# Kernel tuning notes

Hardware: AMD Instinct MI355X
Metric: run time of the kernel (lower is better)

## Reference

```python
import jax, jax.numpy as jnp
import numpy as np

H, W, S = 480, 1024, 32
MULT_THRESH, ADD_THRESH = 0.01, 0.1


def setup_inputs() -> dict:
    key = jax.random.key(0)
    k1, k2 = jax.random.split(key)
    flows_f = jax.random.normal(k1, (1, S, 2, H, W), jnp.float32)
    noise = jax.random.normal(k2, (1, S, 2, H, W), jnp.float32)
    # near-inverse backward flow so the fwd-bwd consistency check passes for many points
    flows_b = -flows_f + 0.05 * noise
    return {"flows_f": flows_f, "flows_b": flows_b, "margin": 10, "sample_step": 4}


def bilinear_sample(im, x, y):
    # im: (C,H,W); x,y: (N,) float pixel coords -> (C,N). Matches torch bilinear_sample2d
    # (weights from unclipped coords, gather indices clipped to the image).
    C, Hh, Ww = im.shape
    x0 = jnp.floor(x); y0 = jnp.floor(y)
    wx1 = x - x0; wx0 = 1.0 - wx1
    wy1 = y - y0; wy0 = 1.0 - wy1
    x0i = jnp.clip(x0.astype(jnp.int32), 0, Ww - 1)
    x1i = jnp.clip(x0i + 1, 0, Ww - 1)
    y0i = jnp.clip(y0.astype(jnp.int32), 0, Hh - 1)
    y1i = jnp.clip(y0i + 1, 0, Hh - 1)
    g = lambda yi, xi: im[:, yi, xi]  # (C,N)
    return (g(y0i, x0i) * (wy0 * wx0) + g(y0i, x1i) * (wy0 * wx1)
            + g(y1i, x0i) * (wy1 * wx0) + g(y1i, x1i) * (wy1 * wx1))


def _forward(ff, fb, margin, sample_step):
    # ff, fb: (S, 2, H, W) forward / backward flows (batch squeezed, B=1)
    gy = jnp.arange(margin, H - margin + 1, sample_step, dtype=jnp.float32)
    gx = jnp.arange(margin, W - margin + 1, sample_step, dtype=jnp.float32)
    YY, XX = jnp.meshgrid(gy, gx, indexing='ij')
    ys_g = YY.reshape(-1); xs_g = XX.reshape(-1)          # (G,) base sampling grid
    G = xs_g.shape[0]
    N = 2 * H * W // (sample_step ** 2)                   # trajectory slot capacity
    R = min(N, G)                                         # max births per step (static)

    by, bx = jnp.meshgrid(jnp.arange(H, dtype=jnp.float32),
                          jnp.arange(W, dtype=jnp.float32), indexing='ij')

    def prune(flow_f, flow_b):
        # fwd-bwd consistency mask 'on': (H,W) in {0,1}
        xt = (bx + flow_f[0]).reshape(-1)
        yt = (by + flow_f[1]).reshape(-1)
        fbw = bilinear_sample(flow_b, xt, yt).reshape(2, H, W)  # backwarped bwd flow
        diff = jnp.sqrt(jnp.sum((flow_f + fbw) ** 2, axis=0))
        mag = 0.5 * (jnp.sqrt(jnp.sum(flow_f ** 2, axis=0)) + jnp.sqrt(jnp.sum(fbw ** 2, axis=0)))
        return (diff <= MULT_THRESH * mag + ADD_THRESH).astype(jnp.float32)

    X = jnp.zeros((S, N), jnp.float32)
    Y = jnp.zeros((S, N), jnp.float32)
    Start = -jnp.ones((N,), jnp.float32)
    X = X.at[0, :G].set(xs_g)
    Y = Y.at[0, :G].set(ys_g)
    Start = Start.at[:G].set(0.0)

    def step(carry, inp):
        X, Y, Start = carry
        flow_f, flow_b, s = inp
        on = prune(flow_f, flow_b)                         # (H,W)
        active = Start >= 0.0                              # (N,) live-slot mask (replaces where(Start>=0))
        xs_o = X[s]; ys_o = Y[s]
        uv = bilinear_sample(flow_f, xs_o, ys_o)           # (2,N) flow at current points
        xs_t = xs_o + uv[0]; ys_t = ys_o + uv[1]
        fb_ok = bilinear_sample(on[None], xs_o, ys_o)[0] > 0.5
        marg = ((xs_t > margin) & (ys_t > margin) &
                (xs_t < W - margin) & (ys_t < H - margin))
        choose = active & marg & fb_ok
        # scatter surviving points into row s+1 (row starts as zeros, matching init)
        X = X.at[s + 1].set(jnp.where(choose, xs_t, 0.0))
        Y = Y.at[s + 1].set(jnp.where(choose, ys_t, 0.0))
        Start = jnp.where(active & ~choose, -1.0, Start)   # terminated slots freed
        # occupancy map of surviving targets, dilated by 5x5 ones-conv (== maxpool on binary)
        oy = jnp.where(choose, ys_t, jnp.float32(H)).astype(jnp.int32)
        ox = jnp.where(choose, xs_t, jnp.float32(W)).astype(jnp.int32)
        occ = jnp.zeros((H, W), jnp.float32).at[oy, ox].set(1.0, mode='drop')
        occ = jax.lax.reduce_window(occ, 0.0, jax.lax.max, (5, 5), (1, 1), 'SAME')
        map_occ = bilinear_sample(occ[None], xs_g, ys_g)[0]
        free_cand = (1.0 - map_occ) == 1.0                 # (G,) unoccupied grid points
        # compaction without dynamic shapes: stable-sort free-first, keep original order
        cand_order = jnp.argsort(~free_cand, stable=True)  # free candidates first
        num_cand = jnp.sum(free_cand)
        free_slot = Start < 0.0
        slot_order = jnp.argsort(~free_slot, stable=True)  # free slots first
        num_free = jnp.sum(free_slot)
        m = jnp.minimum(num_cand, num_free)
        r = jnp.arange(R)
        tgt = jnp.where(r < m, slot_order[:R], N)          # index N -> dropped
        X = X.at[s + 1, tgt].set(xs_g[cand_order[:R]], mode='drop')
        Y = Y.at[s + 1, tgt].set(ys_g[cand_order[:R]], mode='drop')
        Start = Start.at[tgt].set((s + 1).astype(jnp.float32), mode='drop')
        return (X, Y, Start), None

    steps = jnp.arange(S - 1)
    (X, Y, Start), _ = jax.lax.scan(step, (X, Y, Start), (ff[:-1], fb[:-1], steps))
    return jnp.stack([X, Y]), Start


def reference(flows_f, flows_b, margin, sample_step):
    # Returns dense trajectory buffers XY: (2, S, N) and final Start: (N,)
    # (the ragged python-list trajectory extraction is a host-side post-process).
    return _forward(flows_f[0], flows_b[0], margin, sample_step)
```

## Files before the change

kernel.cpp:

```cpp
#include <hip/hip_runtime.h>
#include <cstdint>

#define HH 480
#define WW 1024
#define SS 32
#define HW (HH*WW)
#define MARGIN 10
#define STEP 4
#define GYC 116
#define GXC 252
#define GG (GYC*GXC)
#define NSLOT (2*HH*WW/(STEP*STEP))
#define NBLK (NSLOT/256)
#define NWAVE (NSLOT/64)
#define CW ((GG+63)/64)
#define CWP 512
#define OCCB (CW*64)
#define FS 64
#define FP (256*FS)

__device__ __forceinline__ unsigned int aload(const unsigned int* p) {
  return __hip_atomic_load(p, __ATOMIC_RELAXED, __HIP_MEMORY_SCOPE_AGENT);
}
__device__ __forceinline__ void astore(unsigned int* p, unsigned int v) {
  __hip_atomic_store(p, v, __ATOMIC_RELAXED, __HIP_MEMORY_SCOPE_AGENT);
}
__device__ __forceinline__ unsigned long long aload64(const unsigned long long* p) {
  return __hip_atomic_load(p, __ATOMIC_RELAXED, __HIP_MEMORY_SCOPE_AGENT);
}
__device__ __forceinline__ void astore64(unsigned long long* p, unsigned long long v) {
  __hip_atomic_store(p, v, __ATOMIC_RELAXED, __HIP_MEMORY_SCOPE_AGENT);
}
__device__ __forceinline__ void astore8(unsigned char* p, unsigned char v) {
  __hip_atomic_store(p, v, __ATOMIC_RELAXED, __HIP_MEMORY_SCOPE_AGENT);
}

__device__ __forceinline__ int clampi(int v, int lo, int hi) {
  return v < lo ? lo : (v > hi ? hi : v);
}

__global__ __launch_bounds__(256) void k_init(unsigned int* __restrict__ flags,
                                              unsigned int* __restrict__ occ32)
{
  int idx = blockIdx.x * 256 + threadIdx.x;
  if (idx < (2 * OCCB / 4)) occ32[idx] = 0u;
  if (idx < 256) {
    unsigned v = (idx < NBLK) ? 0u : 0x7FFFFFFFu;
    flags[idx * FS] = v;
    flags[FP + idx * FS] = v;
  }
}

__device__ __forceinline__ int barrier_ps(unsigned int* flagbase, int epoch,
                                          int myblk, int* psB, const int* wcnt)
{
  __syncthreads();
  if (threadIdx.x == 0) {
    int c = wcnt[0] + wcnt[1] + wcnt[2] + wcnt[3];
    astore(&flagbase[myblk * FS], ((unsigned)epoch << 9) | (unsigned)c);
  }
  if (threadIdx.x < 64) {
    const int lane = threadIdx.x;
    unsigned v0, v1, v2, v3;
    for (;;) {
      v0 = aload(&flagbase[(lane      ) * FS]);
      v1 = aload(&flagbase[(lane +  64) * FS]);
      v2 = aload(&flagbase[(lane + 128) * FS]);
      v3 = aload(&flagbase[(lane + 192) * FS]);
      unsigned m0 = v0 >> 9, m1 = v1 >> 9, m2 = v2 >> 9, m3 = v3 >> 9;
      unsigned mn = m0 < m1 ? m0 : m1;
      unsigned mn2 = m2 < m3 ? m2 : m3;
      mn = mn < mn2 ? mn : mn2;
      for (int o = 32; o > 0; o >>= 1) {
        unsigned t = (unsigned)__shfl_xor((int)mn, o, 64);
        mn = mn < t ? mn : t;
      }
      if ((int)mn >= epoch) break;
      __builtin_amdgcn_s_sleep(1);
    }
    int acc = 0;
    if (lane       < myblk) acc += (int)(v0 & 511u);
    if (lane +  64 < myblk) acc += (int)(v1 & 511u);
    if (lane + 128 < myblk) acc += (int)(v2 & 511u);
    if (lane + 192 < myblk) acc += (int)(v3 & 511u);
    for (int o = 32; o > 0; o >>= 1) acc += __shfl_xor(acc, o, 64);
    if (lane == 0) *psB = acc;
  }
  __syncthreads();
  return *psB;
}

struct Bil {
  int x0i, x1i, y0i, y1i;
  int i00, i01, i10, i11;
  float w00, w01, w10, w11;
};

__device__ __forceinline__ Bil mkbil(float xs, float ys) {
#pragma clang fp contract(off)
  float x0 = floorf(xs), y0 = floorf(ys);
  float wx1 = xs - x0, wx0 = 1.0f - wx1;
  float wy1 = ys - y0, wy0 = 1.0f - wy1;
  Bil b;
  b.x0i = clampi((int)x0, 0, WW - 1);
  b.x1i = b.x0i + 1 > WW - 1 ? WW - 1 : b.x0i + 1;
  b.y0i = clampi((int)y0, 0, HH - 1);
  b.y1i = b.y0i + 1 > HH - 1 ? HH - 1 : b.y0i + 1;
  b.i00 = b.y0i * WW + b.x0i; b.i01 = b.y0i * WW + b.x1i;
  b.i10 = b.y1i * WW + b.x0i; b.i11 = b.y1i * WW + b.x1i;
  b.w00 = wy0 * wx0; b.w01 = wy0 * wx1;
  b.w10 = wy1 * wx0; b.w11 = wy1 * wx1;
  return b;
}

__device__ __forceinline__ float prune_val(float fx, float fy,
    float c00a, float c01a, float c10a, float c11a,
    float c00b, float c01b, float c10b, float c11b, const Bil& t)
{
#pragma clang fp contract(off)
  float bw0 = ((c00a * t.w00 + c01a * t.w01) + c10a * t.w10) + c11a * t.w11;
  float bw1 = ((c00b * t.w00 + c01b * t.w01) + c10b * t.w10) + c11b * t.w11;
  float t0 = fx + bw0, t1 = fy + bw1;
  float diff = sqrtf(t0 * t0 + t1 * t1);
  float magf = sqrtf(fx * fx + fy * fy);
  float magb = sqrtf(bw0 * bw0 + bw1 * bw1);
  float mag = 0.5f * (magf + magb);
  return (diff <= 0.01f * mag + 0.1f) ? 1.0f : 0.0f;
}

__device__ __forceinline__ unsigned long long make_intadv(
    int pix, int piy, float fx, float fy, const float* __restrict__ bks)
{
#pragma clang fp contract(off)
  float xt = (float)pix + fx, yt = (float)piy + fy;
  Bil Bt = mkbil(xt, yt);
  const float* b0p = bks;
  const float* b1p = bks + HW;
  float o = prune_val(fx, fy,
                      b0p[Bt.i00], b0p[Bt.i01], b0p[Bt.i10], b0p[Bt.i11],
                      b1p[Bt.i00], b1p[Bt.i01], b1p[Bt.i10], b1p[Bt.i11], Bt);
  bool marg = (xt > (float)MARGIN) && (yt > (float)MARGIN) &&
              (xt < (float)(WW - MARGIN)) && (yt < (float)(HH - MARGIN));
  bool ch = marg && (o > 0.5f);
  unsigned lo = __float_as_uint(ch ? xt : 0.0f);
  unsigned hi = __float_as_uint(ch ? yt : -1.0f);
  return ((unsigned long long)hi << 32) | (unsigned long long)lo;
}

__global__ __launch_bounds__(256, 1) void k_steps(
    const float* __restrict__ ff, const float* __restrict__ fbk,
    float* __restrict__ X, float* __restrict__ Y, float* __restrict__ Start,
    unsigned char* __restrict__ occ, unsigned int* __restrict__ flags,
    unsigned long long* __restrict__ intadv)
{
#pragma clang fp contract(off)
  const int tid = blockIdx.x * 256 + threadIdx.x;
  const int lane = tid & 63;
  const int wv = threadIdx.x >> 6;
  const unsigned long long ltmask = (1ull << lane) - 1ull;

  __shared__ unsigned long long wds[CWP];
  __shared__ unsigned int pref[CWP];
  __shared__ int wsum[4];
  __shared__ int wcnt[4];
  __shared__ int psB;

  float x = 0.f, y = 0.f, st = -1.f;
  int mode = 0;
  float pf0 = 0.f, pf1 = 0.f, pf2 = 0.f, pf3 = 0.f;
  float pf4 = 0.f, pf5 = 0.f, pf6 = 0.f, pf7 = 0.f;
  float pb[32];
  float pxt = 0.f, pyt = 0.f;
  bool  pmarg = false;
  unsigned long long pa64 = (unsigned long long)0xBF800000u << 32;

  const bool prod = (tid < GG);
  int pix = 0, piy = 0, pp = 0;
  float fNx = 0.f, fNy = 0.f;
  float fCx = 0.f, fCy = 0.f;
  float bC0 = 0.f, bC1 = 0.f, bC2 = 0.f, bC3 = 0.f;
  float bC4 = 0.f, bC5 = 0.f, bC6 = 0.f, bC7 = 0.f;

  if (prod) {
    int ii = tid / GXC, jj = tid - ii * GXC;
    pix = MARGIN + STEP * jj; piy = MARGIN + STEP * ii;
    pp = piy * WW + pix;
    x = (float)pix; y = (float)piy;
    st = 0.f; mode = 2;
  }
  X[tid] = x; Y[tid] = y;

  if (prod) {
    float f1x = ff[(size_t)1 * 2 * HW + pp], f1y = ff[(size_t)1 * 2 * HW + HW + pp];
    float f2x = ff[(size_t)2 * 2 * HW + pp], f2y = ff[(size_t)2 * 2 * HW + HW + pp];
    float f3x = ff[(size_t)3 * 2 * HW + pp], f3y = ff[(size_t)3 * 2 * HW + HW + pp];
    fNx = ff[(size_t)4 * 2 * HW + pp];       fNy = ff[(size_t)4 * 2 * HW + HW + pp];
    float f0x = ff[pp],                      f0y = ff[HW + pp];
    pa64 = make_intadv(pix, piy, f0x, f0y, fbk);
    astore64(&intadv[(size_t)1 * GG + tid],
             make_intadv(pix, piy, f1x, f1y, fbk + (size_t)1 * 2 * HW));
    astore64(&intadv[(size_t)2 * GG + tid],
             make_intadv(pix, piy, f2x, f2y, fbk + (size_t)2 * 2 * HW));
    {
      float xt = (float)pix + f3x, yt = (float)piy + f3y;
      Bil Bt = mkbil(xt, yt);
      const float* bb0 = fbk + (size_t)3 * 2 * HW;
      const float* bb1 = bb0 + HW;
      bC0 = bb0[Bt.i00]; bC1 = bb0[Bt.i01]; bC2 = bb0[Bt.i10]; bC3 = bb0[Bt.i11];
      bC4 = bb1[Bt.i00]; bC5 = bb1[Bt.i01]; bC6 = bb1[Bt.i10]; bC7 = bb1[Bt.i11];
      fCx = f3x; fCy = f3y;
    }
  }

#define ISSUE_TAP(tt, TXI, TYI, FX, FY) do { \
    Bil Bt = mkbil((float)P.TXI + (FX), (float)P.TYI + (FY)); \
    pb[(tt)*8+0] = b0n[Bt.i00]; pb[(tt)*8+1] = b0n[Bt.i01]; \
    pb[(tt)*8+2] = b0n[Bt.i10]; pb[(tt)*8+3] = b0n[Bt.i11]; \
    pb[(tt)*8+4] = b1n[Bt.i00]; pb[(tt)*8+5] = b1n[Bt.i01]; \
    pb[(tt)*8+6] = b1n[Bt.i10]; pb[(tt)*8+7] = b1n[Bt.i11]; \
  } while (0)

#define PRUNE_TAP(tt, TXI, TYI, FX, FY, OUT) do { \
    Bil Bt = mkbil((float)P.TXI + (FX), (float)P.TYI + (FY)); \
    OUT = prune_val((FX), (FY), \
                    pb[(tt)*8+0], pb[(tt)*8+1], pb[(tt)*8+2], pb[(tt)*8+3], \
                    pb[(tt)*8+4], pb[(tt)*8+5], pb[(tt)*8+6], pb[(tt)*8+7], Bt); \
  } while (0)

  for (int s = 0; s < SS - 1; ++s) {
    const float* f0n = ff + (size_t)(s + 1) * 2 * HW;
    const float* f1n = f0n + HW;
    const unsigned char tag = (unsigned char)(s + 1);
    unsigned char* occw = occ + (((s + 1) & 1) ? OCCB : 0);

    bool moved = false;
    if (mode == 1) {
      Bil P = mkbil(x, y);
      float o0, o1, o2, o3;
      PRUNE_TAP(0, x0i, y0i, pf0, pf4, o0);
      PRUNE_TAP(1, x1i, y0i, pf1, pf5, o1);
      PRUNE_TAP(2, x0i, y1i, pf2, pf6, o2);
      PRUNE_TAP(3, x1i, y1i, pf3, pf7, o3);
      float fbv = ((o0 * P.w00 + o1 * P.w01) + o2 * P.w10) + o3 * P.w11;
      if (pmarg && fbv > 0.5f) {
        x = pxt; y = pyt;
        Bil Pn = mkbil(x, y);
        pf0 = f0n[Pn.i00]; pf1 = f0n[Pn.i01]; pf2 = f0n[Pn.i10]; pf3 = f0n[Pn.i11];
        pf4 = f1n[Pn.i00]; pf5 = f1n[Pn.i01]; pf6 = f1n[Pn.i10]; pf7 = f1n[Pn.i11];
        moved = true;
      } else { st = -1.f; x = 0.f; y = 0.f; mode = 0; }
    } else if (mode == 2) {
      float axt = __uint_as_float((unsigned)pa64);
      float ayt = __uint_as_float((unsigned)(pa64 >> 32));
      if (ayt >= 0.0f) {
        x = axt; y = ayt; mode = 1;
        Bil Pn = mkbil(x, y);
        pf0 = f0n[Pn.i00]; pf1 = f0n[Pn.i01]; pf2 = f0n[Pn.i10]; pf3 = f0n[Pn.i11];
        pf4 = f1n[Pn.i00]; pf5 = f1n[Pn.i01]; pf6 = f1n[Pn.i10]; pf7 = f1n[Pn.i11];
        moved = true;
      } else { st = -1.f; x = 0.f; y = 0.f; mode = 0; }
    }
    if (moved) {
      int oy = (int)y, ox = (int)x;
      int i0 = ((oy - (MARGIN + 2) + 4099) >> 2) - 1024;
      int i1 = ((oy - (MARGIN - 2) + 4096) >> 2) - 1024;
      int j0 = ((ox - (MARGIN + 2) + 4099) >> 2) - 1024;
      int j1 = ((ox - (MARGIN - 2) + 4096) >> 2) - 1024;
      if (i0 < 0) i0 = 0; if (i1 > GYC - 1) i1 = GYC - 1;
      if (j0 < 0) j0 = 0; if (j1 > GXC - 1) j1 = GXC - 1;
      for (int i = i0; i <= i1; ++i)
        for (int j = j0; j <= j1; ++j)
          astore8(&occw[i * GXC + j], tag);
    }
    unsigned long long smask = __ballot(st < 0.0f);
    if (lane == 0) wcnt[wv] = (int)__popcll(smask);

    int ps = barrier_ps(flags + (s & 1) * FP, s + 1, blockIdx.x, &psB, wcnt);

    unsigned long long cv[16];
    {
      const unsigned long long* occ64 =
          (const unsigned long long*)(occ + (((s + 1) & 1) ? OCCB : 0));
      int t = threadIdx.x;
#pragma unroll
      for (int r = 0; r < 16; ++r) {
        int j = t + 256 * r;
        cv[r] = (j < GG / 8) ? aload64(&occ64[j]) : 0ull;
      }
    }
    if (mode == 1 && s < SS - 2) {
      Bil P = mkbil(x, y);
      float u_ = ((pf0 * P.w00 + pf1 * P.w01) + pf2 * P.w10) + pf3 * P.w11;
      float v_ = ((pf4 * P.w00 + pf5 * P.w01) + pf6 * P.w10) + pf7 * P.w11;
      pxt = x + u_; pyt = y + v_;
      pmarg = (pxt > (float)MARGIN) && (pyt > (float)MARGIN) &&
              (pxt < (float)(WW - MARGIN)) && (pyt < (float)(HH - MARGIN));
      const float* b0n = fbk + (size_t)(s + 1) * 2 * HW;
      const float* b1n = b0n + HW;
      ISSUE_TAP(0, x0i, y0i, pf0, pf4);
      ISSUE_TAP(1, x1i, y0i, pf1, pf5);
      ISSUE_TAP(2, x0i, y1i, pf2, pf6);
      ISSUE_TAP(3, x1i, y1i, pf3, pf7);
    }
    if (prod) {
      if (s <= SS - 5) {
        float xt = (float)pix + fCx, yt = (float)piy + fCy;
        Bil Bt = mkbil(xt, yt);
        float o = prune_val(fCx, fCy, bC0, bC1, bC2, bC3, bC4, bC5, bC6, bC7, Bt);
        bool marg = (xt > (float)MARGIN) && (yt > (float)MARGIN) &&
                    (xt < (float)(WW - MARGIN)) && (yt < (float)(HH - MARGIN));
        bool ch = marg && (o > 0.5f);
        unsigned lo = __float_as_uint(ch ? xt : 0.0f);
        unsigned hi = __float_as_uint(ch ? yt : -1.0f);
        astore64(&intadv[(size_t)(s + 3) * GG + tid],
                 ((unsigned long long)hi << 32) | (unsigned long long)lo);
      }
      if (s <= SS - 6) {
        float xt = (float)pix + fNx, yt = (float)piy + fNy;
        Bil Bt = mkbil(xt, yt);
        const float* bb0 = fbk + (size_t)(s + 4) * 2 * HW;
        const float* bb1 = bb0 + HW;
        bC0 = bb0[Bt.i00]; bC1 = bb0[Bt.i01]; bC2 = bb0[Bt.i10]; bC3 = bb0[Bt.i11];
        bC4 = bb1[Bt.i00]; bC5 = bb1[Bt.i01]; bC6 = bb1[Bt.i10]; bC7 = bb1[Bt.i11];
        fCx = fNx; fCy = fNy;
      }
      if (s <= SS - 7) {
        const float* fp_ = ff + (size_t)(s + 5) * 2 * HW;
        fNx = fp_[pp]; fNy = fp_[HW + pp];
      }
    }
    {
      unsigned char* nb = (unsigned char*)wds;
      const unsigned long long tr = 0x0101010101010101ull * (unsigned long long)tag;
      int t = threadIdx.x;
#pragma unroll
      for (int r = 0; r < 16; ++r) {
        int j = t + 256 * r;
        unsigned long long xx = cv[r] ^ tr;
        unsigned long long t1 = (xx & 0x7F7F7F7F7F7F7F7Full) + 0x7F7F7F7F7F7F7F7Full;
        unsigned long long nz = ((t1 | xx) >> 7) & 0x0101010101010101ull;
        unsigned char byte = (unsigned char)((nz * 0x0102040810204080ull) >> 56);
        nb[j] = (j < GG / 8) ? byte : (unsigned char)0;
      }
    }
    __syncthreads();
    {
      int t = threadIdx.x;
      int e0 = 2 * t, e1 = 2 * t + 1;
      unsigned long long m0 = wds[e0];
      unsigned long long m1 = wds[e1];
      int p0 = __popcll(m0), p1 = __popcll(m1);
      int v = p0 + p1;
      for (int o = 1; o < 64; o <<= 1) {
        int uu = __shfl_up(v, o, 64);
        if (lane >= o) v += uu;
      }
      if (lane == 63) wsum[wv] = v;
      __syncthreads();
      int base = 0;
      for (int j2 = 0; j2 < wv; ++j2) base += wsum[j2];
      pref[e0] = (unsigned int)(base + v - p1);
      pref[e1] = (unsigned int)(base + v);
      __syncthreads();
    }
    int tc = (int)pref[CWP - 1];

    int lower = 0;
    for (int j2 = 0; j2 < wv; ++j2) lower += wcnt[j2];

    if (st < 0.0f) {
      int r = ps + lower + (int)__popcll(smask & ltmask);
      if (r < tc) {
        int k = 0;
        for (int b = 256; b >= 1; b >>= 1) {
          int nk = k + b;
          if (nk <= CWP - 1 && (int)pref[nk - 1] <= r) k = nk;
        }
        int j = r - (k ? (int)pref[k - 1] : 0);
        unsigned long long m = wds[k];
        int lo = 0;
        for (int b = 32; b >= 1; b >>= 1) {
          int nb = lo + b;
          unsigned long long mask = (nb >= 64) ? ~0ull : ((1ull << nb) - 1ull);
          if (__popcll(m & mask) <= j) lo = nb;
        }
        int g = k * 64 + lo;
        int ii = g / GXC, jj = g - ii * GXC;
        x = (float)(MARGIN + STEP * jj);
        y = (float)(MARGIN + STEP * ii);
        st = (float)(s + 1);
        mode = 2;
        if (s < SS - 2)
          pa64 = aload64(&intadv[(size_t)(s + 1) * GG + g]);
      }
    }
    X[(size_t)(s + 1) * NSLOT + tid] = x;
    Y[(size_t)(s + 1) * NSLOT + tid] = y;
    __syncthreads();
  }

#undef ISSUE_TAP
#undef PRUNE_TAP

  Start[tid] = st;
}

extern "C" void kernel_launch(void* const* d_in, const int* in_sizes, int n_in,
                              void* d_out, int out_size, void* d_ws, size_t ws_size,
                              hipStream_t stream) {
  const float* ff  = (const float*)d_in[0];
  const float* fbk = (const float*)d_in[1];

  float* X     = (float*)d_out;
  float* Y     = X + (size_t)SS * NSLOT;
  float* Start = Y + (size_t)SS * NSLOT;

  unsigned int*       flags  = (unsigned int*)d_ws;
  unsigned char*      occ    = (unsigned char*)(flags + 2 * FP);
  unsigned long long* intadv = (unsigned long long*)(occ + 2 * OCCB);

  k_init<<<58, 256, 0, stream>>>(flags, (unsigned int*)occ);

  k_steps<<<NBLK, 256, 0, stream>>>(ff, fbk, X, Y, Start, occ, flags, intadv);
}
```

Measured before the change: 431.6 us.

## Interleave slot-to-wave mapping, balance producer cells per block, per-wave barrier prefix sums

Slots are now assigned so that each wave of a block takes a strided chunk across all blocks, and producer (intadv precompute) work is spread evenly as every other thread over CPB cells per block, instead of sitting in the first blocks. The grid barrier now publishes per-wave counts packed into a 64-bit flag and computes per-wave exclusive prefixes directly. The trailing per-step __syncthreads is dropped by double-buffering wcnt. The aim is to balance the producer load and the trajectory workload across CUs and to shorten the serial critical path of each grid barrier. The cost is more complex bit packing and counts limited to 8 bits each.

```diff
diff --git a/kernel.cpp b/kernel.cpp
--- a/kernel.cpp
+++ b/kernel.cpp
@@ -16,8 +16,9 @@
 #define CW ((GG+63)/64)
 #define CWP 512
 #define OCCB (CW*64)
-#define FS 64
-#define FP (256*FS)
+#define FS8 32
+#define FP8 (256*FS8)
+#define CPB 122
 
 __device__ __forceinline__ unsigned int aload(const unsigned int* p) {
   return __hip_atomic_load(p, __ATOMIC_RELAXED, __HIP_MEMORY_SCOPE_AGENT);
@@ -39,35 +40,38 @@
   return v < lo ? lo : (v > hi ? hi : v);
 }
 
-__global__ __launch_bounds__(256) void k_init(unsigned int* __restrict__ flags,
+__global__ __launch_bounds__(256) void k_init(unsigned long long* __restrict__ flags,
                                               unsigned int* __restrict__ occ32)
 {
   int idx = blockIdx.x * 256 + threadIdx.x;
   if (idx < (2 * OCCB / 4)) occ32[idx] = 0u;
   if (idx < 256) {
-    unsigned v = (idx < NBLK) ? 0u : 0x7FFFFFFFu;
-    flags[idx * FS] = v;
-    flags[FP + idx * FS] = v;
-  }
-}
-
-__device__ __forceinline__ int barrier_ps(unsigned int* flagbase, int epoch,
-                                          int myblk, int* psB, const int* wcnt)
+    unsigned long long v = (idx < NBLK) ? 0ull : (0x7FFFFFFFull << 32);
+    flags[idx * FS8] = v;
+    flags[FP8 + idx * FS8] = v;
+  }
+}
+
+__device__ __forceinline__ void barrier_ps4(unsigned long long* flagbase, int epoch,
+                                            int myblk, int* ps4, const int* wcnt)
 {
   __syncthreads();
   if (threadIdx.x == 0) {
-    int c = wcnt[0] + wcnt[1] + wcnt[2] + wcnt[3];
-    astore(&flagbase[myblk * FS], ((unsigned)epoch << 9) | (unsigned)c);
+    unsigned cpack = (unsigned)wcnt[0] | ((unsigned)wcnt[1] << 8)
+                   | ((unsigned)wcnt[2] << 16) | ((unsigned)wcnt[3] << 24);
+    astore64(&flagbase[myblk * FS8],
+             ((unsigned long long)(unsigned)epoch << 32) | (unsigned long long)cpack);
   }
   if (threadIdx.x < 64) {
     const int lane = threadIdx.x;
-    unsigned v0, v1, v2, v3;
+    unsigned long long v0, v1, v2, v3;
     for (;;) {
-      v0 = aload(&flagbase[(lane      ) * FS]);
-      v1 = aload(&flagbase[(lane +  64) * FS]);
-      v2 = aload(&flagbase[(lane + 128) * FS]);
-      v3 = aload(&flagbase[(lane + 192) * FS]);
-      unsigned m0 = v0 >> 9, m1 = v1 >> 9, m2 = v2 >> 9, m3 = v3 >> 9;
+      v0 = aload64(&flagbase[(lane      ) * FS8]);
+      v1 = aload64(&flagbase[(lane +  64) * FS8]);
+      v2 = aload64(&flagbase[(lane + 128) * FS8]);
+      v3 = aload64(&flagbase[(lane + 192) * FS8]);
+      unsigned m0 = (unsigned)(v0 >> 32), m1 = (unsigned)(v1 >> 32);
+      unsigned m2 = (unsigned)(v2 >> 32), m3 = (unsigned)(v3 >> 32);
       unsigned mn = m0 < m1 ? m0 : m1;
       unsigned mn2 = m2 < m3 ? m2 : m3;
       mn = mn < mn2 ? mn : mn2;
@@ -78,16 +82,40 @@
       if ((int)mn >= epoch) break;
       __builtin_amdgcn_s_sleep(1);
     }
-    int acc = 0;
-    if (lane       < myblk) acc += (int)(v0 & 511u);
-    if (lane +  64 < myblk) acc += (int)(v1 & 511u);
-    if (lane + 128 < myblk) acc += (int)(v2 & 511u);
-    if (lane + 192 < myblk) acc += (int)(v3 & 511u);
-    for (int o = 32; o > 0; o >>= 1) acc += __shfl_xor(acc, o, 64);
-    if (lane == 0) *psB = acc;
+    auto up = [](unsigned long long f) -> unsigned long long {
+      unsigned c = (unsigned)f;
+      return (unsigned long long)(c & 0xFFu)
+           | ((unsigned long long)((c >>  8) & 0xFFu) << 16)
+           | ((unsigned long long)((c >> 16) & 0xFFu) << 32)
+           | ((unsigned long long)((c >> 24) & 0xFFu) << 48);
+    };
+    unsigned long long u0 = up(v0), u1 = up(v1), u2 = up(v2), u3 = up(v3);
+    unsigned long long F = u0 + u1 + u2 + u3;
+    unsigned long long P = (lane       < myblk ? u0 : 0ull)
+                         + (lane +  64 < myblk ? u1 : 0ull)
+                         + (lane + 128 < myblk ? u2 : 0ull)
+                         + (lane + 192 < myblk ? u3 : 0ull);
+    for (int o = 32; o > 0; o >>= 1) {
+      unsigned flo = (unsigned)F, fhi = (unsigned)(F >> 32);
+      unsigned plo = (unsigned)P, phi = (unsigned)(P >> 32);
+      unsigned flo2 = (unsigned)__shfl_xor((int)flo, o, 64);
+      unsigned fhi2 = (unsigned)__shfl_xor((int)fhi, o, 64);
+      unsigned plo2 = (unsigned)__shfl_xor((int)plo, o, 64);
+      unsigned phi2 = (unsigned)__shfl_xor((int)phi, o, 64);
+      F += ((unsigned long long)fhi2 << 32) | flo2;
+      P += ((unsigned long long)phi2 << 32) | plo2;
+    }
+    if (lane == 0) {
+      int f0 = (int)(F & 0xFFFF), f1 = (int)((F >> 16) & 0xFFFF), f2 = (int)((F >> 32) & 0xFFFF);
+      int p0 = (int)(P & 0xFFFF), p1 = (int)((P >> 16) & 0xFFFF);
+      int p2 = (int)((P >> 32) & 0xFFFF), p3 = (int)((P >> 48) & 0xFFFF);
+      ps4[0] = p0;
+      ps4[1] = f0 + p1;
+      ps4[2] = f0 + f1 + p2;
+      ps4[3] = f0 + f1 + f2 + p3;
+    }
   }
   __syncthreads();
-  return *psB;
 }
 
 struct Bil {
@@ -150,20 +178,21 @@
 __global__ __launch_bounds__(256, 1) void k_steps(
     const float* __restrict__ ff, const float* __restrict__ fbk,
     float* __restrict__ X, float* __restrict__ Y, float* __restrict__ Start,
-    unsigned char* __restrict__ occ, unsigned int* __restrict__ flags,
+    unsigned char* __restrict__ occ, unsigned long long* __restrict__ flags,
     unsigned long long* __restrict__ intadv)
 {
 #pragma clang fp contract(off)
-  const int tid = blockIdx.x * 256 + threadIdx.x;
-  const int lane = tid & 63;
+  const int b = blockIdx.x;
+  const int lane = threadIdx.x & 63;
   const int wv = threadIdx.x >> 6;
+  const int slot = ((wv * NBLK + b) << 6) | lane;
   const unsigned long long ltmask = (1ull << lane) - 1ull;
 
   __shared__ unsigned long long wds[CWP];
   __shared__ unsigned int pref[CWP];
   __shared__ int wsum[4];
-  __shared__ int wcnt[4];
-  __shared__ int psB;
+  __shared__ int wcnt[2][4];
+  __shared__ int ps4[4];
 
   float x = 0.f, y = 0.f, st = -1.f;
   int mode = 0;
@@ -174,32 +203,37 @@
   bool  pmarg = false;
   unsigned long long pa64 = (unsigned long long)0xBF800000u << 32;
 
-  const bool prod = (tid < GG);
+  const int pj = threadIdx.x >> 1;
+  const int pcell = b * CPB + pj;
+  const bool prod = ((threadIdx.x & 1) == 0) && (pj < CPB) && (pcell < GG);
   int pix = 0, piy = 0, pp = 0;
   float fNx = 0.f, fNy = 0.f;
   float fCx = 0.f, fCy = 0.f;
   float bC0 = 0.f, bC1 = 0.f, bC2 = 0.f, bC3 = 0.f;
   float bC4 = 0.f, bC5 = 0.f, bC6 = 0.f, bC7 = 0.f;
 
+  if (slot < GG) {
+    int ii = slot / GXC, jj = slot - ii * GXC;
+    int ix = MARGIN + STEP * jj, iy = MARGIN + STEP * ii;
+    x = (float)ix; y = (float)iy;
+    st = 0.f; mode = 2;
+    int p0_ = iy * WW + ix;
+    float f0x = ff[p0_], f0y = ff[HW + p0_];
+    pa64 = make_intadv(ix, iy, f0x, f0y, fbk);
+  }
+  X[slot] = x; Y[slot] = y;
+
   if (prod) {
-    int ii = tid / GXC, jj = tid - ii * GXC;
+    int ii = pcell / GXC, jj = pcell - ii * GXC;
     pix = MARGIN + STEP * jj; piy = MARGIN + STEP * ii;
     pp = piy * WW + pix;
-    x = (float)pix; y = (float)piy;
-    st = 0.f; mode = 2;
-  }
-  X[tid] = x; Y[tid] = y;
-
-  if (prod) {
     float f1x = ff[(size_t)1 * 2 * HW + pp], f1y = ff[(size_t)1 * 2 * HW + HW + pp];
     float f2x = ff[(size_t)2 * 2 * HW + pp], f2y = ff[(size_t)2 * 2 * HW + HW + pp];
     float f3x = ff[(size_t)3 * 2 * HW + pp], f3y = ff[(size_t)3 * 2 * HW + HW + pp];
     fNx = ff[(size_t)4 * 2 * HW + pp];       fNy = ff[(size_t)4 * 2 * HW + HW + pp];
-    float f0x = ff[pp],                      f0y = ff[HW + pp];
-    pa64 = make_intadv(pix, piy, f0x, f0y, fbk);
-    astore64(&intadv[(size_t)1 * GG + tid],
+    astore64(&intadv[(size_t)1 * GG + pcell],
              make_intadv(pix, piy, f1x, f1y, fbk + (size_t)1 * 2 * HW));
-    astore64(&intadv[(size_t)2 * GG + tid],
+    astore64(&intadv[(size_t)2 * GG + pcell],
              make_intadv(pix, piy, f2x, f2y, fbk + (size_t)2 * 2 * HW));
     {
       float xt = (float)pix + f3x, yt = (float)piy + f3y;
@@ -273,9 +307,10 @@
           astore8(&occw[i * GXC + j], tag);
     }
     unsigned long long smask = __ballot(st < 0.0f);
-    if (lane == 0) wcnt[wv] = (int)__popcll(smask);
-
-    int ps = barrier_ps(flags + (s & 1) * FP, s + 1, blockIdx.x, &psB, wcnt);
+    if (lane == 0) wcnt[s & 1][wv] = (int)__popcll(smask);
+
+    barrier_ps4(flags + (s & 1) * FP8, s + 1, b, ps4, wcnt[s & 1]);
+    int ps = ps4[wv];
 
     unsigned long long cv[16];
     {
@@ -312,7 +347,7 @@
         bool ch = marg && (o > 0.5f);
         unsigned lo = __float_as_uint(ch ? xt : 0.0f);
         unsigned hi = __float_as_uint(ch ? yt : -1.0f);
-        astore64(&intadv[(size_t)(s + 3) * GG + tid],
+        astore64(&intadv[(size_t)(s + 3) * GG + pcell],
                  ((unsigned long long)hi << 32) | (unsigned long long)lo);
       }
       if (s <= SS - 6) {
@@ -365,24 +400,21 @@
     }
     int tc = (int)pref[CWP - 1];
 
-    int lower = 0;
-    for (int j2 = 0; j2 < wv; ++j2) lower += wcnt[j2];
-
     if (st < 0.0f) {
-      int r = ps + lower + (int)__popcll(smask & ltmask);
+      int r = ps + (int)__popcll(smask & ltmask);
       if (r < tc) {
         int k = 0;
-        for (int b = 256; b >= 1; b >>= 1) {
-          int nk = k + b;
+        for (int bb = 256; bb >= 1; bb >>= 1) {
+          int nk = k + bb;
           if (nk <= CWP - 1 && (int)pref[nk - 1] <= r) k = nk;
         }
         int j = r - (k ? (int)pref[k - 1] : 0);
         unsigned long long m = wds[k];
         int lo = 0;
-        for (int b = 32; b >= 1; b >>= 1) {
-          int nb = lo + b;
-          unsigned long long mask = (nb >= 64) ? ~0ull : ((1ull << nb) - 1ull);
-          if (__popcll(m & mask) <= j) lo = nb;
+        for (int bb = 32; bb >= 1; bb >>= 1) {
+          int nb2 = lo + bb;
+          unsigned long long mask = (nb2 >= 64) ? ~0ull : ((1ull << nb2) - 1ull);
+          if (__popcll(m & mask) <= j) lo = nb2;
         }
         int g = k * 64 + lo;
         int ii = g / GXC, jj = g - ii * GXC;
@@ -394,15 +426,14 @@
           pa64 = aload64(&intadv[(size_t)(s + 1) * GG + g]);
       }
     }
-    X[(size_t)(s + 1) * NSLOT + tid] = x;
-    Y[(size_t)(s + 1) * NSLOT + tid] = y;
-    __syncthreads();
+    X[(size_t)(s + 1) * NSLOT + slot] = x;
+    Y[(size_t)(s + 1) * NSLOT + slot] = y;
   }
 
 #undef ISSUE_TAP
 #undef PRUNE_TAP
 
-  Start[tid] = st;
+  Start[slot] = st;
 }
 
 extern "C" void kernel_launch(void* const* d_in, const int* in_sizes, int n_in,
@@ -415,8 +446,8 @@
   float* Y     = X + (size_t)SS * NSLOT;
   float* Start = Y + (size_t)SS * NSLOT;
 
-  unsigned int*       flags  = (unsigned int*)d_ws;
-  unsigned char*      occ    = (unsigned char*)(flags + 2 * FP);
+  unsigned long long* flags  = (unsigned long long*)d_ws;
+  unsigned char*      occ    = (unsigned char*)(flags + 2 * FP8);
   unsigned long long* intadv = (unsigned long long*)(occ + 2 * OCCB);
 
   k_init<<<58, 256, 0, stream>>>(flags, (unsigned int*)occ);
```

After: 428.6 us. No clear change (-0.7%).
